# Kernel optimization log

Measured on AMD Instinct MI355X. Metric: run time of the kernel, lower is better.

## Reference

```python
import jax, jax.numpy as jnp
import numpy as np

N_NODES = 50000
N_EDGES = 800000
IN_F = 128
OUT_F = 256


def setup_inputs() -> dict:
    key = jax.random.key(0)
    k1, k2, k3, k4, k5, k6 = jax.random.split(key, 6)
    x = jax.random.normal(k1, (N_NODES, IN_F), dtype=jnp.float32)
    edge_row = jax.random.randint(k2, (N_EDGES,), 0, N_NODES, dtype=jnp.int32)
    edge_col = jax.random.randint(k3, (N_EDGES,), 0, N_NODES, dtype=jnp.int32)
    edge_val = jax.random.uniform(k4, (N_EDGES,), dtype=jnp.float32)
    weight = jax.random.normal(k5, (IN_F, OUT_F), dtype=jnp.float32) * (1.0 / np.sqrt(OUT_F))
    b = jax.random.normal(k6, (OUT_F,), dtype=jnp.float32) * 0.01
    return {"x": x, "edge_row": edge_row, "edge_col": edge_col,
            "edge_val": edge_val, "weight": weight, "b": b}


def reference(x, edge_row, edge_col, edge_val, weight, b):
    # spmm: agg[i] = sum_{e: row[e]==i} val[e] * x[col[e]]
    msgs = edge_val[:, None] * x[edge_col]              # [E, in_f]
    agg = jax.ops.segment_sum(msgs, edge_row, num_segments=x.shape[0])  # [N, in_f]
    # dense transform + bias
    return agg @ weight + b                              # [N, out_f]
```

## Files before the change

kernel.cpp:

```cpp
#include <hip/hip_runtime.h>
#include <hip/hip_bf16.h>

#define N_NODES 50000
#define N_EDGES 800000
#define IN_F    128
#define OUT_F   256

typedef __attribute__((ext_vector_type(8))) short  short8;
typedef __attribute__((ext_vector_type(4))) float  f32x4;

static __device__ __forceinline__ unsigned short f2bf(float f) {
    __hip_bfloat16 h = __float2bfloat16(f);
    return *reinterpret_cast<unsigned short*>(&h);
}


__global__ __launch_bounds__(256)
void convert_x(const float* __restrict__ x, unsigned short* __restrict__ xb, int n8) {
    const int i = blockIdx.x * blockDim.x + threadIdx.x;
    if (i >= n8) return;
    const float4* xp = reinterpret_cast<const float4*>(x) + (size_t)i * 2;
    const float4 a = xp[0], b = xp[1];
    uint4 o;
    o.x = (unsigned)f2bf(a.x) | ((unsigned)f2bf(a.y) << 16);
    o.y = (unsigned)f2bf(a.z) | ((unsigned)f2bf(a.w) << 16);
    o.z = (unsigned)f2bf(b.x) | ((unsigned)f2bf(b.y) << 16);
    o.w = (unsigned)f2bf(b.z) | ((unsigned)f2bf(b.w) << 16);
    reinterpret_cast<uint4*>(xb)[i] = o;
}

__global__ __launch_bounds__(256)
void convert_w(const float* __restrict__ W, unsigned short* __restrict__ Wt) {
    const int n  = blockIdx.x * 16 + (threadIdx.x & 15);
    const int kc = threadIdx.x >> 4;
    unsigned q[4];
#pragma unroll
    for (int j = 0; j < 4; ++j) {
        const int k = kc * 8 + j * 2;
        const unsigned short u0 = f2bf(W[(size_t)k * OUT_F + n]);
        const unsigned short u1 = f2bf(W[(size_t)(k + 1) * OUT_F + n]);
        q[j] = (unsigned)u0 | ((unsigned)u1 << 16);
    }
    *reinterpret_cast<uint4*>(Wt + (size_t)n * IN_F + kc * 8) =
        make_uint4(q[0], q[1], q[2], q[3]);
}

__global__ __launch_bounds__(256)
void hist_rank(const int* __restrict__ row, int* __restrict__ cnt,
               int* __restrict__ rank, int E) {
    int e = blockIdx.x * blockDim.x + threadIdx.x;
    if (e < E) rank[e] = atomicAdd(&cnt[row[e]], 1);
}

#define SCAN_BLK 1024

__global__ __launch_bounds__(SCAN_BLK)
void scan_block(const int* __restrict__ cnt, int* __restrict__ rptr,
                int* __restrict__ bsum, int n) {
    __shared__ int s[SCAN_BLK];
    const int gid = blockIdx.x * SCAN_BLK + threadIdx.x;
    const int v = (gid < n) ? cnt[gid] : 0;
    s[threadIdx.x] = v;
    __syncthreads();
    for (int d = 1; d < SCAN_BLK; d <<= 1) {
        int t = (threadIdx.x >= d) ? s[threadIdx.x - d] : 0;
        __syncthreads();
        s[threadIdx.x] += t;
        __syncthreads();
    }
    const int incl = s[threadIdx.x];
    if (gid < n) rptr[gid] = incl - v;
    if (threadIdx.x == SCAN_BLK - 1) bsum[blockIdx.x] = incl;
}

__global__ __launch_bounds__(64)
void scan_top(int* __restrict__ bsum, int nb) {
    const int lane = threadIdx.x;
    int v = (lane < nb) ? bsum[lane] : 0;
    for (int d = 1; d < 64; d <<= 1) {
        int u = __shfl_up(v, d);
        if (lane >= d) v += u;
    }
    int ex = __shfl_up(v, 1);
    if (lane == 0) ex = 0;
    if (lane < nb) bsum[lane] = ex;
}

__global__ __launch_bounds__(SCAN_BLK)
void scan_add(int* __restrict__ rptr, const int* __restrict__ bsum, int n) {
    const int gid = blockIdx.x * SCAN_BLK + threadIdx.x;
    if (gid < n) rptr[gid] += bsum[blockIdx.x];
}

__global__ __launch_bounds__(256)
void edge_fill(const int* __restrict__ row, const int* __restrict__ col,
               const float* __restrict__ val,
               const int* __restrict__ rptr, const int* __restrict__ rank,
               unsigned long long* __restrict__ recs, int E) {
    int e = blockIdx.x * blockDim.x + threadIdx.x;
    if (e >= E) return;
    const int r = row[e];
    const int p = rptr[r] + rank[e];
    const unsigned long long rec =
        ((unsigned long long)__float_as_uint(val[e]) << 32) | (unsigned)col[e];
    recs[p] = rec;
}

__global__ __launch_bounds__(256)
void gather_agg(const unsigned short* __restrict__ xb,
                const int* __restrict__ rptr,
                const int* __restrict__ cnt,
                const unsigned long long* __restrict__ recs,
                float* __restrict__ out, int M) {
    const int wave = threadIdx.x >> 6;
    const int lane = threadIdx.x & 63;
    const int node = blockIdx.x * 4 + wave;
    if (node >= M) return;

    const int es = lane >> 3;
    const int fg = lane & 7;

    const int st = rptr[node];
    const int d  = cnt[node];

    float acc[16];
#pragma unroll
    for (int i = 0; i < 16; ++i) acc[i] = 0.f;

    for (int j0 = 0; j0 < d; j0 += 8) {
        const int  idx = j0 + es;
        const bool ok  = (idx < d);
        const unsigned long long rec = recs[st + (ok ? idx : 0)];
        const int   c = (int)(unsigned)(rec & 0xffffffffull);
        const float v = ok ? __uint_as_float((unsigned)(rec >> 32)) : 0.f;

        const uint4* xp = reinterpret_cast<const uint4*>(
            xb + (size_t)c * IN_F + fg * 16);
        const uint4 a = xp[0], b = xp[1];
        const unsigned w[8] = {a.x, a.y, a.z, a.w, b.x, b.y, b.z, b.w};
#pragma unroll
        for (int j = 0; j < 8; ++j) {
            acc[2 * j]     += v * __uint_as_float(w[j] << 16);
            acc[2 * j + 1] += v * __uint_as_float(w[j] & 0xffff0000u);
        }
    }

#pragma unroll
    for (int i = 0; i < 16; ++i) {
        acc[i] += __shfl_xor(acc[i], 8);
        acc[i] += __shfl_xor(acc[i], 16);
        acc[i] += __shfl_xor(acc[i], 32);
    }

    if (es == 0) {
        unsigned q[8];
#pragma unroll
        for (int j = 0; j < 8; ++j)
            q[j] = (unsigned)f2bf(acc[2 * j]) | ((unsigned)f2bf(acc[2 * j + 1]) << 16);
        unsigned short* op =
            reinterpret_cast<unsigned short*>(out) + (size_t)node * 512 + fg * 16;
        reinterpret_cast<uint4*>(op)[0] = make_uint4(q[0], q[1], q[2], q[3]);
        reinterpret_cast<uint4*>(op)[1] = make_uint4(q[4], q[5], q[6], q[7]);
    }
}

__global__ __launch_bounds__(256)
void gemm_mfma(const unsigned short* __restrict__ Wt,
               const float* __restrict__ bias,
               float* __restrict__ out, int M) {
    const int tid = threadIdx.x;
    const int wv  = tid >> 6;
    const int l   = tid & 63;
    const int wvm = wv >> 1, wvn = wv & 1;
    const int lr  = l & 15;
    const int lg  = l >> 4;
    const int r0  = blockIdx.x * 64;

    short8 af[2][4];
#pragma unroll
    for (int mt = 0; mt < 2; ++mt) {
        const int row = r0 + wvm * 32 + mt * 16 + lr;
        const unsigned short* ap =
            reinterpret_cast<const unsigned short*>(out) + (size_t)row * 512;
#pragma unroll
        for (int kk = 0; kk < 4; ++kk) {
            short8 v = {0, 0, 0, 0, 0, 0, 0, 0};
            if (row < M)
                v = *reinterpret_cast<const short8*>(ap + kk * 32 + lg * 8);
            af[mt][kk] = v;
        }
    }
    __syncthreads();

    f32x4 acc[2][8];
#pragma unroll
    for (int mt = 0; mt < 2; ++mt)
#pragma unroll
        for (int nt = 0; nt < 8; ++nt) acc[mt][nt] = (f32x4){0.f, 0.f, 0.f, 0.f};

#pragma unroll
    for (int kk = 0; kk < 4; ++kk) {
        short8 bf[8];
#pragma unroll
        for (int nt = 0; nt < 8; ++nt) {
            const int colc = wvn * 128 + nt * 16 + lr;
            bf[nt] = *reinterpret_cast<const short8*>(
                Wt + (size_t)colc * IN_F + kk * 32 + lg * 8);
        }
#pragma unroll
        for (int mt = 0; mt < 2; ++mt)
#pragma unroll
            for (int nt = 0; nt < 8; ++nt)
                acc[mt][nt] = __builtin_amdgcn_mfma_f32_16x16x32_bf16(
                    af[mt][kk], bf[nt], acc[mt][nt], 0, 0, 0);
    }

#pragma unroll
    for (int nt = 0; nt < 8; ++nt) {
        const int colc = wvn * 128 + nt * 16 + lr;
        const float bv = bias[colc];
#pragma unroll
        for (int mt = 0; mt < 2; ++mt) {
            const int rbase = r0 + wvm * 32 + mt * 16 + lg * 4;
#pragma unroll
            for (int r = 0; r < 4; ++r) {
                const int gr = rbase + r;
                if (gr < M)
                    out[(size_t)gr * OUT_F + colc] = acc[mt][nt][r] + bv;
            }
        }
    }
}

extern "C" void kernel_launch(void* const* d_in, const int* in_sizes, int n_in,
                              void* d_out, int out_size, void* d_ws, size_t ws_size,
                              hipStream_t stream) {
    const float* x        = (const float*)d_in[0];
    const int*   edge_row = (const int*)  d_in[1];
    const int*   edge_col = (const int*)  d_in[2];
    const float* edge_val = (const float*)d_in[3];
    const float* weight   = (const float*)d_in[4];
    const float* bias     = (const float*)d_in[5];
    float* out = (float*)d_out;

    char* w = (char*)d_ws;
    unsigned short* xb = (unsigned short*)w;
    unsigned long long* recs = (unsigned long long*)(w + 12800000);
    unsigned short* Wt = (unsigned short*)(w + 19200000);
    int* cnt  = (int*)(w + 19265536);
    int* rptr = cnt + 50000;
    int* bsum = rptr + 50000;
    int* rank = bsum + 64;

    hipMemsetAsync(cnt, 0, (size_t)N_NODES * sizeof(int), stream);

    convert_x<<<(N_NODES * IN_F / 8 + 255) / 256, 256, 0, stream>>>(
        x, xb, N_NODES * IN_F / 8);
    convert_w<<<16, 256, 0, stream>>>(weight, Wt);

    const int nscan = (N_NODES + SCAN_BLK - 1) / SCAN_BLK;
    hist_rank<<<(N_EDGES + 255) / 256, 256, 0, stream>>>(edge_row, cnt, rank, N_EDGES);
    scan_block<<<nscan, SCAN_BLK, 0, stream>>>(cnt, rptr, bsum, N_NODES);
    scan_top<<<1, 64, 0, stream>>>(bsum, nscan);
    scan_add<<<nscan, SCAN_BLK, 0, stream>>>(rptr, bsum, N_NODES);
    edge_fill<<<(N_EDGES + 255) / 256, 256, 0, stream>>>(
        edge_row, edge_col, edge_val, rptr, rank, recs, N_EDGES);

    gather_agg<<<(N_NODES + 3) / 4, 256, 0, stream>>>(
        xb, rptr, cnt, recs, out, N_NODES);

    gemm_mfma<<<(N_NODES + 63) / 64, 256, 0, stream>>>(
        Wt, bias, out, N_NODES);
}
```

Baseline: 219.4 us.

## Restructure GEMM so each wave owns 16 rows and writes float4 outputs

Each wave now computes a full 16x256 output slab for its own 16 rows, instead of a 2x2 wave grid that split rows and columns. Swapping the MFMA operands (W as A, activations as B) makes each lane hold four consecutive output columns of one row, so results go out as 128-bit float4 stores with a vectorized bias load, replacing scattered scalar stores. This also removes the __syncthreads, which protected the in-place overwrite of the bf16 agg buffer that aliases the output, because each wave now only reads and writes its own rows. The cost is that W is re-read per wave for every column tile and there is less register reuse across rows.

```diff
diff --git a/kernel.cpp b/kernel.cpp
--- a/kernel.cpp
+++ b/kernel.cpp
@@ -171,63 +171,45 @@
     const int tid = threadIdx.x;
     const int wv  = tid >> 6;
     const int l   = tid & 63;
-    const int wvm = wv >> 1, wvn = wv & 1;
     const int lr  = l & 15;
     const int lg  = l >> 4;
-    const int r0  = blockIdx.x * 64;
-
-    short8 af[2][4];
-#pragma unroll
-    for (int mt = 0; mt < 2; ++mt) {
-        const int row = r0 + wvm * 32 + mt * 16 + lr;
-        const unsigned short* ap =
-            reinterpret_cast<const unsigned short*>(out) + (size_t)row * 512;
-#pragma unroll
-        for (int kk = 0; kk < 4; ++kk) {
-            short8 v = {0, 0, 0, 0, 0, 0, 0, 0};
-            if (row < M)
-                v = *reinterpret_cast<const short8*>(ap + kk * 32 + lg * 8);
-            af[mt][kk] = v;
-        }
-    }
-    __syncthreads();
-
-    f32x4 acc[2][8];
-#pragma unroll
-    for (int mt = 0; mt < 2; ++mt)
-#pragma unroll
-        for (int nt = 0; nt < 8; ++nt) acc[mt][nt] = (f32x4){0.f, 0.f, 0.f, 0.f};
-
+    const int row0 = blockIdx.x * 64 + wv * 16;
+
+    const int arow = row0 + lr;
+    const unsigned short* ap =
+        reinterpret_cast<const unsigned short*>(out) + (size_t)arow * 512;
+    short8 af[4];
 #pragma unroll
     for (int kk = 0; kk < 4; ++kk) {
-        short8 bf[8];
-#pragma unroll
-        for (int nt = 0; nt < 8; ++nt) {
-            const int colc = wvn * 128 + nt * 16 + lr;
-            bf[nt] = *reinterpret_cast<const short8*>(
-                Wt + (size_t)colc * IN_F + kk * 32 + lg * 8);
-        }
-#pragma unroll
-        for (int mt = 0; mt < 2; ++mt)
-#pragma unroll
-            for (int nt = 0; nt < 8; ++nt)
-                acc[mt][nt] = __builtin_amdgcn_mfma_f32_16x16x32_bf16(
-                    af[mt][kk], bf[nt], acc[mt][nt], 0, 0, 0);
-    }
-
-#pragma unroll
-    for (int nt = 0; nt < 8; ++nt) {
-        const int colc = wvn * 128 + nt * 16 + lr;
-        const float bv = bias[colc];
-#pragma unroll
-        for (int mt = 0; mt < 2; ++mt) {
-            const int rbase = r0 + wvm * 32 + mt * 16 + lg * 4;
-#pragma unroll
-            for (int r = 0; r < 4; ++r) {
-                const int gr = rbase + r;
-                if (gr < M)
-                    out[(size_t)gr * OUT_F + colc] = acc[mt][nt][r] + bv;
-            }
+        short8 v = {0, 0, 0, 0, 0, 0, 0, 0};
+        if (arow < M)
+            v = *reinterpret_cast<const short8*>(ap + kk * 32 + lg * 8);
+        af[kk] = v;
+    }
+
+    const int crow = row0 + lr;
+    float* orow = out + (size_t)crow * OUT_F;
+
+#pragma unroll 2
+    for (int nt = 0; nt < 16; ++nt) {
+        const int wcol = nt * 16 + lr;
+        short8 wf[4];
+#pragma unroll
+        for (int kk = 0; kk < 4; ++kk)
+            wf[kk] = *reinterpret_cast<const short8*>(
+                Wt + (size_t)wcol * IN_F + kk * 32 + lg * 8);
+
+        f32x4 acc = (f32x4){0.f, 0.f, 0.f, 0.f};
+#pragma unroll
+        for (int kk = 0; kk < 4; ++kk)
+            acc = __builtin_amdgcn_mfma_f32_16x16x32_bf16(
+                wf[kk], af[kk], acc, 0, 0, 0);
+
+        const float4 bv = *reinterpret_cast<const float4*>(bias + nt * 16 + lg * 4);
+        if (crow < M) {
+            const float4 o = make_float4(acc[0] + bv.x, acc[1] + bv.y,
+                                         acc[2] + bv.z, acc[3] + bv.w);
+            *reinterpret_cast<float4*>(orow + nt * 16 + lg * 4) = o;
         }
     }
 }
```

New measurement: 221.2 us. About the same (+0.8%).
